# Kernel optimization log

Hardware: AMD Instinct MI355X
Metric: run time of the kernel (lower is better)

Reference implementation:

```python
import jax, jax.numpy as jnp
import numpy as np

T, B, N, C, H, D = 4, 8, 1024, 512, 8, 64
EPS = 1e-5


def setup_inputs() -> dict:
    key = jax.random.key(0)
    ks = jax.random.split(key, 16)
    d = {"x": jax.random.normal(ks[0], (T, B, N, C), jnp.float32)}
    for i, nm in enumerate(["q", "k", "v", "p"]):
        kW, kmu, kvar = jax.random.split(ks[1 + i], 3)
        d[f"W{nm}"] = jax.random.normal(kW, (C, C), jnp.float32) * 0.02
        d[f"b{nm}"] = jnp.zeros((C,), jnp.float32)
        d[f"g{nm}"] = jnp.ones((C,), jnp.float32)
        d[f"beta{nm}"] = jnp.zeros((C,), jnp.float32)
        d[f"mu{nm}"] = jax.random.normal(kmu, (C,), jnp.float32) * 0.1
        d[f"var{nm}"] = jax.random.uniform(kvar, (C,), jnp.float32, 0.5, 1.5)
    return d


def _lin_bn(z, W, b, g, beta, mu, var):
    # nn.Linear over channel dim, then eval-mode BatchNorm1d per channel
    y = jnp.einsum('tbnc,dc->tbnd', z, W) + b
    return (y - mu) * (g * jax.lax.rsqrt(var + EPS)) + beta


def _to_heads(z):
    # (t,b,n,c) -> (t,b,h,n,d)
    return z.reshape(T, B, N, H, D).transpose(0, 1, 3, 2, 4)


def reference(x, Wq, bq, gq, betaq, muq, varq,
              Wk, bk, gk, betak, muk, vark,
              Wv, bv, gv, betav, muv, varv,
              Wp, bp, gp, betap, mup, varp):
    q = _to_heads(_lin_bn(x, Wq, bq, gq, betaq, muq, varq))
    k = _to_heads(_lin_bn(x, Wk, bk, gk, betak, muk, vark))
    v = _to_heads(_lin_bn(x, Wv, bv, gv, betav, muv, varv))
    # attention_linear variant: kv = (k^T @ v) / N ; y = q @ kv
    kv = jnp.einsum('tbhnd,tbhne->tbhde', k, v) / float(N)  # (t,b,h,d,d)
    y = jnp.einsum('tbhnd,tbhde->tbhne', q, kv)             # (t,b,h,n,d)
    y = y.transpose(0, 1, 3, 2, 4).reshape(T, B, N, C)
    return _lin_bn(y, Wp, bp, gp, betap, mup, varp)
```

## Files before the change

### kernel.cpp

```cpp
#include <hip/hip_runtime.h>

#define T_ 4
#define B_ 8
#define N_ 1024
#define C_ 512
#define H_ 8
#define D_ 64
#define M_ (T_*B_*N_)
#define TB_ (T_*B_)

typedef __bf16 bf16;
typedef __bf16 bf16x4 __attribute__((ext_vector_type(4)));
typedef __bf16 bf16x8 __attribute__((ext_vector_type(8)));
typedef float f32x4 __attribute__((ext_vector_type(4)));

__device__ __forceinline__ void gload16(const void* g, void* l) {
  __builtin_amdgcn_global_load_lds(
      (const __attribute__((address_space(1))) void*)g,
      (__attribute__((address_space(3))) void*)l, 16, 0, 0);
}

struct PtrPack { const float* p[24]; };

__global__ __launch_bounds__(256)
void prep_m(PtrPack pk, bf16* __restrict__ WB, float* __restrict__ BS,
            bf16* __restrict__ WqT) {
  const int t = threadIdx.x;
  if (blockIdx.x < 2048) {
    const int mat = blockIdx.x >> 9, d = blockIdx.x & 511;
    const float* W    = pk.p[6*mat + 0];
    const float* b    = pk.p[6*mat + 1];
    const float* g    = pk.p[6*mat + 2];
    const float* beta = pk.p[6*mat + 3];
    const float* mu   = pk.p[6*mat + 4];
    const float* var  = pk.p[6*mat + 5];
    float s = g[d] * rsqrtf(var[d] + 1e-5f);
    if (t == 0) BS[mat*512 + d] = (b[d] - mu[d]) * s + beta[d];
    bf16* Wout = WB + (size_t)mat * 262144 + (size_t)d * 512;
    for (int c = t; c < 512; c += 256)
      Wout[c] = (bf16)(W[(size_t)d * 512 + c] * s);
    return;
  }
  const int e = blockIdx.x - 2048;
  const int di = e >> 3, ci = e & 7;
  __shared__ float lds[64][65];
  const float* W = pk.p[0];
  const float* g = pk.p[2];
  const float* var = pk.p[5];
  const int rgrp = t >> 4, k = t & 15;
#pragma unroll
  for (int p = 0; p < 4; p++) {
    int r = p * 16 + rgrp;
    int d = di * 64 + r;
    float s = g[d] * rsqrtf(var[d] + 1e-5f);
    float4 v = *(const float4*)(W + (size_t)d * 512 + ci * 64 + k * 4);
    lds[r][k*4+0] = v.x * s; lds[r][k*4+1] = v.y * s;
    lds[r][k*4+2] = v.z * s; lds[r][k*4+3] = v.w * s;
  }
  __syncthreads();
#pragma unroll
  for (int p = 0; p < 16; p++) {
    int c = p * 4 + (t >> 6), dd = t & 63;
    WqT[(size_t)(ci*64 + c) * 512 + di*64 + dd] = (bf16)lds[dd][c];
  }
}

__global__ __launch_bounds__(256)
void cvt_x_t(const float* __restrict__ x, bf16* __restrict__ xb,
             bf16* __restrict__ xT, float* __restrict__ spart) {
  const int bid = blockIdx.x;
  const int tb = bid >> 7, nc = (bid >> 3) & 15, cc = bid & 7;
  const int t = threadIdx.x;
  __shared__ float lds[64][65];
  __shared__ float sred[16][64];
  const float* xbase = x + (size_t)tb * 524288 + (size_t)nc * 64 * 512 + cc * 64;
  bf16* xbb = xb + (size_t)tb * 524288 + (size_t)nc * 64 * 512 + cc * 64;
  bf16* xTb = xT + (size_t)tb * 524288 + (size_t)(cc * 64) * 1024 + nc * 64;
  const int rgrp = t >> 4, k = t & 15;
  float s0 = 0, s1 = 0, s2 = 0, s3 = 0;
#pragma unroll
  for (int p = 0; p < 4; p++) {
    int r = p * 16 + rgrp;
    float4 v = *(const float4*)(xbase + (size_t)r * 512 + k * 4);
    bf16x4 o; o[0]=(bf16)v.x; o[1]=(bf16)v.y; o[2]=(bf16)v.z; o[3]=(bf16)v.w;
    *(bf16x4*)(xbb + (size_t)r * 512 + k * 4) = o;
    lds[r][k*4+0]=v.x; lds[r][k*4+1]=v.y; lds[r][k*4+2]=v.z; lds[r][k*4+3]=v.w;
    s0 += v.x; s1 += v.y; s2 += v.z; s3 += v.w;
  }
  sred[rgrp][k*4+0]=s0; sred[rgrp][k*4+1]=s1; sred[rgrp][k*4+2]=s2; sred[rgrp][k*4+3]=s3;
  __syncthreads();
#pragma unroll
  for (int p = 0; p < 16; p++) {
    int c = p * 4 + (t >> 6), n = t & 63;
    xTb[(size_t)c * 1024 + n] = (bf16)lds[n][c];
  }
  if (t < 64) {
    float tot = 0;
#pragma unroll
    for (int rg = 0; rg < 16; rg++) tot += sred[rg][t];
    spart[(size_t)((tb*8 + cc)*16 + nc) * 64 + t] = tot;
  }
}

__global__ __launch_bounds__(256)
void gram_ksvs(const bf16* __restrict__ xT, const bf16* __restrict__ WB,
               const float* __restrict__ spart, bf16* __restrict__ Gb,
               float* __restrict__ ksv) {
  const int t = threadIdx.x;
  __shared__ __align__(16) char smem[24576];
  if (blockIdx.x >= 640) {
    const int e = blockIdx.x - 640, tb = e >> 1, m = e & 1;
    float* sl = (float*)smem;
#pragma unroll
    for (int half = 0; half < 2; half++) {
      int c = t + half * 256, cc = c >> 6, cl = c & 63;
      float tot = 0;
#pragma unroll
      for (int ncf = 0; ncf < 16; ncf++)
        tot += spart[(size_t)((tb*8 + cc)*16 + ncf) * 64 + cl];
      sl[c] = tot;
    }
    __syncthreads();
#pragma unroll
    for (int half = 0; half < 2; half++) {
      int d = t + half * 256;
      const bf16* Wrow = WB + (size_t)(m + 1) * 262144 + (size_t)d * 512;
      float acc = 0;
      for (int k = 0; k < 512; k += 8) {
        bf16x8 wv = *(const bf16x8*)(Wrow + k);
#pragma unroll
        for (int i = 0; i < 8; i++) acc += (float)wv[i] * sl[k + i];
      }
      ksv[m * 16384 + tb * 512 + d] = acc;
    }
    return;
  }
  constexpr int K = 1024;
  const int bid = blockIdx.x;
  const int xcd = bid & 7, j9 = bid >> 3;
  const int bat = xcd + 8 * (j9 / 20);
  const int tile = j9 % 20;
  int mi, ni;
  if (tile < 8)       { mi = tile;          ni = 0; }
  else if (tile < 14) { mi = tile - 8 + 2;  ni = 1; }
  else if (tile < 18) { mi = tile - 14 + 4; ni = 2; }
  else                { mi = tile - 18 + 6; ni = 3; }
  const bf16* A = xT + (size_t)bat * 524288;
  const int m0 = mi * 64, n0 = ni * 128;
  bf16* As = (bf16*)smem;
  bf16* Bs = (bf16*)(smem + 8192);
  const int w = t >> 6, l = t & 63;
  const int wm = w >> 1, wn = w & 1;
  const int lr = l & 15, lq = l >> 4, l7 = l & 7, lh = l >> 3;
  const int srcc = (l7 ^ lh) * 8;
  f32x4 acc[2][4] = {};
  for (int kt = 0; kt < 16; kt++) {
#pragma unroll
    for (int i = 0; i < 2; i++) {
      int rb = w * 16 + i * 8;
      gload16(A + (size_t)(m0 + rb + lh) * K + kt * 64 + srcc, &As[rb * 64]);
    }
#pragma unroll
    for (int i = 0; i < 4; i++) {
      int rb = w * 32 + i * 8;
      gload16(A + (size_t)(n0 + rb + lh) * K + kt * 64 + srcc, &Bs[rb * 64]);
    }
    __syncthreads();
    bf16x8 af[2][2], bv[4][2];
#pragma unroll
    for (int f = 0; f < 2; f++) {
      int ra = wm * 32 + f * 16 + lr;
#pragma unroll
      for (int s = 0; s < 2; s++)
        af[f][s] = *(const bf16x8*)&As[ra * 64 + (((s*4+lq) ^ (ra & 7)) * 8)];
    }
#pragma unroll
    for (int f = 0; f < 4; f++) {
      int rb2 = wn * 64 + f * 16 + lr;
#pragma unroll
      for (int s = 0; s < 2; s++)
        bv[f][s] = *(const bf16x8*)&Bs[rb2 * 64 + (((s*4+lq) ^ (rb2 & 7)) * 8)];
    }
#pragma unroll
    for (int mt = 0; mt < 2; mt++)
#pragma unroll
      for (int nt = 0; nt < 4; nt++)
#pragma unroll
        for (int s = 0; s < 2; s++)
          acc[mt][nt] = __builtin_amdgcn_mfma_f32_16x16x32_bf16(
              af[mt][s], bv[nt][s], acc[mt][nt], 0, 0, 0);
    __syncthreads();
  }
  bf16* ob = Gb + (size_t)bat * 262144;
#pragma unroll
  for (int mt = 0; mt < 2; mt++)
#pragma unroll
    for (int nt = 0; nt < 4; nt++) {
      int j = n0 + wn * 64 + nt * 16 + lr;
      size_t mrow = (size_t)m0 + wm * 32 + mt * 16 + lq * 4;
#pragma unroll
      for (int r = 0; r < 4; r++)
        ob[(mrow + r) * 512 + j] = (bf16)acc[mt][nt][r];
    }
  bf16* TB = (bf16*)smem;
#pragma unroll
  for (int mt = 0; mt < 2; mt++)
#pragma unroll
    for (int nt = 0; nt < 4; nt++) {
      int a = wn * 64 + nt * 16 + lr;
#pragma unroll
      for (int r = 0; r < 4; r++) {
        int b = wm * 32 + mt * 16 + lq * 4 + r;
        TB[(a * 64 + b) ^ ((a & 7) << 3)] = (bf16)acc[mt][nt][r];
      }
    }
  __syncthreads();
  const int rowa = t >> 1, half = t & 1;
#pragma unroll
  for (int i = 0; i < 4; i++) {
    int c8 = half * 4 + i;
    bf16x8 v = *(const bf16x8*)&TB[(rowa * 64 + c8 * 8) ^ ((rowa & 7) << 3)];
    *(bf16x8*)(ob + (size_t)(n0 + rowa) * 512 + m0 + c8 * 8) = v;
  }
}

template <int NKT, int MTILES, bool BF16OUT, bool BIAS>
__global__ __launch_bounds__(256, 6)
void gemm_n(const bf16* __restrict__ Abase, size_t Astr,
            const bf16* __restrict__ Btbase, size_t Btstr,
            const float* __restrict__ BSb, const float* __restrict__ cpart,
            bf16* __restrict__ ob, float* __restrict__ of, size_t Ostr) {
  constexpr int K = NKT * 64;
  constexpr int PERB = MTILES * 4;
  const int bid = blockIdx.x;
  const int xcd = bid & 7, j9 = bid >> 3;
  const int bat = xcd + 8 * (j9 / PERB);
  const int tile = j9 % PERB;
  const int mi = tile >> 2, ni = tile & 3;
  const bf16* A = Abase + (size_t)bat * Astr;
  const bf16* Bt = Btbase + (size_t)bat * Btstr;
  const int m0 = mi * 64, n0 = ni * 128;
  __shared__ __align__(16) bf16 As[64][64];
  __shared__ __align__(16) bf16 Bs[128][64];
  const int tid = threadIdx.x, w = tid >> 6, l = tid & 63;
  const int wm = w >> 1, wn = w & 1;
  const int lr = l & 15, lq = l >> 4, l7 = l & 7, lh = l >> 3;
  const int srcc = (l7 ^ lh) * 8;
  f32x4 acc[2][4] = {};
  for (int kt = 0; kt < NKT; kt++) {
#pragma unroll
    for (int i = 0; i < 2; i++) {
      int rb = w * 16 + i * 8;
      gload16(A + (size_t)(m0 + rb + lh) * K + kt * 64 + srcc, &As[rb][0]);
    }
#pragma unroll
    for (int i = 0; i < 4; i++) {
      int rb = w * 32 + i * 8;
      gload16(Bt + (size_t)(n0 + rb + lh) * K + kt * 64 + srcc, &Bs[rb][0]);
    }
    __syncthreads();
    bf16x8 af[2][2], bv[4][2];
#pragma unroll
    for (int f = 0; f < 2; f++) {
      int ra = wm * 32 + f * 16 + lr;
#pragma unroll
      for (int s = 0; s < 2; s++)
        af[f][s] = *(const bf16x8*)&As[ra][((s*4+lq) ^ (ra & 7)) * 8];
    }
#pragma unroll
    for (int f = 0; f < 4; f++) {
      int rb2 = wn * 64 + f * 16 + lr;
#pragma unroll
      for (int s = 0; s < 2; s++)
        bv[f][s] = *(const bf16x8*)&Bs[rb2][((s*4+lq) ^ (rb2 & 7)) * 8];
    }
#pragma unroll
    for (int mt = 0; mt < 2; mt++)
#pragma unroll
      for (int nt = 0; nt < 4; nt++)
#pragma unroll
        for (int s = 0; s < 2; s++)
          acc[mt][nt] = __builtin_amdgcn_mfma_f32_16x16x32_bf16(
              af[mt][s], bv[nt][s], acc[mt][nt], 0, 0, 0);
    __syncthreads();
  }

  float bja[4];
  if constexpr (BIAS) {
#pragma unroll
    for (int nt = 0; nt < 4; nt++) {
      int j = n0 + wn * 64 + nt * 16 + lr;
      float bj = BSb[1536 + j];
#pragma unroll
      for (int h = 0; h < 8; h++)
        bj += cpart[(size_t)(bat * 8 + h) * 512 + j];
      bja[nt] = bj;
    }
  }
#pragma unroll
  for (int mt = 0; mt < 2; mt++)
#pragma unroll
    for (int nt = 0; nt < 4; nt++) {
      int j = n0 + wn * 64 + nt * 16 + lr;
      size_t mrow = (size_t)m0 + wm * 32 + mt * 16 + lq * 4;
#pragma unroll
      for (int r = 0; r < 4; r++) {
        if constexpr (BF16OUT)
          ob[(size_t)bat * Ostr + (mrow + r) * 512 + j] = (bf16)acc[mt][nt][r];
        else
          of[(size_t)bat * Ostr + (mrow + r) * 512 + j] =
              acc[mt][nt][r] + (BIAS ? bja[nt] : 0.f);
      }
    }
}

__global__ __launch_bounds__(256)
void kvz(const bf16* __restrict__ KGb, const bf16* __restrict__ WB,
         const float* __restrict__ BS, const float* __restrict__ ksv,
         bf16* __restrict__ ZT, float* __restrict__ cpart) {
  const int gid = blockIdx.x, tb = gid >> 3, h = gid & 7;
  const int t = threadIdx.x, w = t >> 6, l = t & 63;
  const int lr = l & 15, lq = l >> 4;
  __shared__ __align__(16) char lds[65536 + 65536 + 8192];
  bf16* bufA = (bf16*)lds;
  bf16* bufV = (bf16*)(lds + 65536);
  bf16* kvb  = (bf16*)(lds + 131072);

#pragma unroll
  for (int i = 0; i < 16; i++) {
    int r = i * 4 + w;
    gload16(KGb + (size_t)tb * 262144 + (size_t)(64*h + r) * 512 + ((l ^ (r & 7)) * 8),
            bufA + r * 512);
    gload16(WB + 2u * 262144 + (size_t)(64*h + r) * 512 + ((l ^ (r & 7)) * 8),
            bufV + r * 512);
  }
  __syncthreads();

  f32x4 acc2[4][4] = {};
#pragma unroll
  for (int ks = 0; ks < 4; ks++) {
    int gch = w * 16 + ks * 4 + lq;
    bf16x8 af2[4], bv2[4];
#pragma unroll
    for (int mf = 0; mf < 4; mf++) {
      int d = mf * 16 + lr;
      af2[mf] = *(const bf16x8*)&bufA[d * 512 + ((gch ^ (d & 7)) * 8)];
    }
#pragma unroll
    for (int nf = 0; nf < 4; nf++) {
      int e = nf * 16 + lr;
      bv2[nf] = *(const bf16x8*)&bufV[e * 512 + ((gch ^ (e & 7)) * 8)];
    }
#pragma unroll
    for (int mf = 0; mf < 4; mf++)
#pragma unroll
      for (int nf = 0; nf < 4; nf++)
        acc2[mf][nf] = __builtin_amdgcn_mfma_f32_16x16x32_bf16(
            af2[mf], bv2[nf], acc2[mf][nf], 0, 0, 0);
  }
  __syncthreads();

  float* part = (float*)lds + w * 4096;
#pragma unroll
  for (int mf = 0; mf < 4; mf++)
#pragma unroll
    for (int nf = 0; nf < 4; nf++)
#pragma unroll
      for (int r = 0; r < 4; r++) {
        int d = mf * 16 + lq * 4 + r, e = nf * 16 + lr;
        part[d * 64 + e] = acc2[mf][nf][r];
      }
  __syncthreads();
  {
    const float inv = 1.f / 1024.f;
    const float* pb = (const float*)lds;
#pragma unroll
    for (int jj = 0; jj < 16; jj++) {
      int flat = jj * 256 + t, d = flat >> 6, e = flat & 63;
      float s = pb[flat] + pb[4096 + flat] + pb[8192 + flat] + pb[12288 + flat];
      float ksh = ksv[tb * 512 + 64*h + d];
      float vsh = ksv[16384 + tb * 512 + 64*h + e];
      float bkh = BS[512 + 64*h + d];
      float bvh = BS[1024 + 64*h + e];
      float kv = (s + ksh * bvh + bkh * vsh) * inv + bkh * bvh;
      kvb[d * 64 + (((e >> 3) ^ (d & 7)) * 8 + (e & 7))] = (bf16)kv;
    }
  }
  __syncthreads();

#pragma unroll
  for (int i = 0; i < 16; i++) {
    int rb = i * 32 + w * 8;
    int r = rb + (l >> 3);
    gload16(WB + 3u * 262144 + (size_t)r * 512 + 64*h + (((l & 7) ^ (r & 7)) * 8),
            bufA + rb * 64);
  }
  __syncthreads();

  f32x4 acc3[4][8] = {};
#pragma unroll
  for (int s = 0; s < 2; s++) {
    bf16x8 af3[4];
#pragma unroll
    for (int mf = 0; mf < 4; mf++) {
      int d = mf * 16 + lr;
      af3[mf] = *(const bf16x8*)&kvb[d * 64 + (((s*4+lq) ^ (d & 7)) * 8)];
    }
#pragma unroll
    for (int nf = 0; nf < 8; nf++) {
      int jj = w * 128 + nf * 16 + lr;
      bf16x8 b3 = *(const bf16x8*)&bufA[jj * 64 + (((s*4+lq) ^ (jj & 7)) * 8)];
#pragma unroll
      for (int mf = 0; mf < 4; mf++)
        acc3[mf][nf] = __builtin_amdgcn_mfma_f32_16x16x32_bf16(
            af3[mf], b3, acc3[mf][nf], 0, 0, 0);
    }
  }

  bf16* zbase = ZT + (size_t)tb * 262144 + 64*h;
#pragma unroll
  for (int nf = 0; nf < 8; nf++) {
    int jj = w * 128 + nf * 16 + lr;
    float cp = 0.f;
#pragma unroll
    for (int mf = 0; mf < 4; mf++) {
      bf16x4 o;
#pragma unroll
      for (int r = 0; r < 4; r++) {
        o[r] = (bf16)acc3[mf][nf][r];
        cp += acc3[mf][nf][r] * BS[64*h + mf*16 + lq*4 + r];
      }
      *(bf16x4*)(zbase + (size_t)jj * 512 + mf * 16 + lq * 4) = o;
    }
    cp += __shfl_xor(cp, 16);
    cp += __shfl_xor(cp, 32);
    if (lq == 0) cpart[(size_t)(tb * 8 + h) * 512 + jj] = cp;
  }
}

extern "C" void kernel_launch(void* const* d_in, const int* in_sizes, int n_in,
                              void* d_out, int out_size, void* d_ws, size_t ws_size,
                              hipStream_t stream) {
  const float* x = (const float*)d_in[0];
  char* ws = (char*)d_ws;
  bf16*  xb    = (bf16*)(ws + 0);
  bf16*  xT    = (bf16*)(ws + 33554432);
  bf16*  Gb    = (bf16*)(ws + 67108864);
  bf16*  KGb   = (bf16*)(ws + 83886080);
  bf16*  ZT    = (bf16*)(ws + 100663296);
  bf16*  VT    = (bf16*)(ws + 117440512);
  bf16*  WB    = (bf16*)(ws + 134217728);
  bf16*  WqT   = (bf16*)(ws + 136314880);
  float* BS    = (float*)(ws + 136839168);
  float* ksv   = (float*)(ws + 136847360);
  float* cpart = (float*)(ws + 136978432);
  float* spart = (float*)(ws + 137502720);
  (void)in_sizes; (void)n_in; (void)out_size; (void)ws_size;

  PtrPack pk;
  for (int i = 0; i < 24; i++) pk.p[i] = (const float*)d_in[1 + i];

  prep_m<<<2112, 256, 0, stream>>>(pk, WB, BS, WqT);
  cvt_x_t<<<4096, 256, 0, stream>>>(x, xb, xT, spart);
  gram_ksvs<<<704, 256, 0, stream>>>(xT, WB, spart, Gb, ksv);
  gemm_n<8, 8, true, false><<<1024, 256, 0, stream>>>(
      WB + 262144, 0, Gb, 262144, nullptr, nullptr, KGb, nullptr, 262144);
  kvz<<<256, 256, 0, stream>>>(KGb, WB, BS, ksv, ZT, cpart);
  gemm_n<8, 8, true, false><<<1024, 256, 0, stream>>>(
      ZT, 262144, WqT, 0, nullptr, nullptr, VT, nullptr, 262144);
  gemm_n<8, 16, false, true><<<2048, 256, 0, stream>>>(
      xb, 524288, VT, 262144, BS, cpart, nullptr, (float*)d_out, 524288);
}
```

Before: 134.6 us.

## Merge prep kernels, precompute output bias vector, and drop LDS staging in kvz

Merges the weight-prep and x-conversion kernels into one launch, which removes a launch and lets the two independent jobs run side by side. Adds a dedicated ZT×WqT GEMM kernel whose extra blocks precompute the per-batch output bias, so the final GEMM reads one bias value per column instead of summing eight partials. kvz now reads K/V and Wp fragments straight from global memory with a different per-wave split, removing large LDS staging and the cross-wave reduction. The cost is uncached strided global reads in kvz, which may lower memory efficiency there.

```diff
diff --git a/kernel.cpp b/kernel.cpp
--- a/kernel.cpp
+++ b/kernel.cpp
@@ -23,11 +23,51 @@
 struct PtrPack { const float* p[24]; };
 
 __global__ __launch_bounds__(256)
-void prep_m(PtrPack pk, bf16* __restrict__ WB, float* __restrict__ BS,
-            bf16* __restrict__ WqT) {
+void cvt_prep(PtrPack pk, const float* __restrict__ x, bf16* __restrict__ xb,
+              bf16* __restrict__ xT, float* __restrict__ spart,
+              bf16* __restrict__ WB, float* __restrict__ BS,
+              bf16* __restrict__ WqT) {
   const int t = threadIdx.x;
-  if (blockIdx.x < 2048) {
-    const int mat = blockIdx.x >> 9, d = blockIdx.x & 511;
+  __shared__ __align__(16) char smem[21120];
+  if (blockIdx.x < 4096) {
+    const int bid = blockIdx.x;
+    const int tb = bid >> 7, nc = (bid >> 3) & 15, cc = bid & 7;
+    float* lds = (float*)smem;
+    float* sred = (float*)smem + 4160;
+    const float* xbase = x + (size_t)tb * 524288 + (size_t)nc * 64 * 512 + cc * 64;
+    bf16* xbb = xb + (size_t)tb * 524288 + (size_t)nc * 64 * 512 + cc * 64;
+    bf16* xTb = xT + (size_t)tb * 524288 + (size_t)(cc * 64) * 1024 + nc * 64;
+    const int rgrp = t >> 4, k = t & 15;
+    float s0 = 0, s1 = 0, s2 = 0, s3 = 0;
+#pragma unroll
+    for (int p = 0; p < 4; p++) {
+      int r = p * 16 + rgrp;
+      float4 v = *(const float4*)(xbase + (size_t)r * 512 + k * 4);
+      bf16x4 o; o[0]=(bf16)v.x; o[1]=(bf16)v.y; o[2]=(bf16)v.z; o[3]=(bf16)v.w;
+      *(bf16x4*)(xbb + (size_t)r * 512 + k * 4) = o;
+      lds[r*65 + k*4+0]=v.x; lds[r*65 + k*4+1]=v.y;
+      lds[r*65 + k*4+2]=v.z; lds[r*65 + k*4+3]=v.w;
+      s0 += v.x; s1 += v.y; s2 += v.z; s3 += v.w;
+    }
+    sred[rgrp*64 + k*4+0]=s0; sred[rgrp*64 + k*4+1]=s1;
+    sred[rgrp*64 + k*4+2]=s2; sred[rgrp*64 + k*4+3]=s3;
+    __syncthreads();
+#pragma unroll
+    for (int p = 0; p < 16; p++) {
+      int c = p * 4 + (t >> 6), n = t & 63;
+      xTb[(size_t)c * 1024 + n] = (bf16)lds[n*65 + c];
+    }
+    if (t < 64) {
+      float tot = 0;
+#pragma unroll
+      for (int rg = 0; rg < 16; rg++) tot += sred[rg*64 + t];
+      spart[(size_t)((tb*8 + cc)*16 + nc) * 64 + t] = tot;
+    }
+    return;
+  }
+  if (blockIdx.x < 6144) {
+    const int e = blockIdx.x - 4096;
+    const int mat = e >> 9, d = e & 511;
     const float* W    = pk.p[6*mat + 0];
     const float* b    = pk.p[6*mat + 1];
     const float* g    = pk.p[6*mat + 2];
@@ -41,9 +81,9 @@
       Wout[c] = (bf16)(W[(size_t)d * 512 + c] * s);
     return;
   }
-  const int e = blockIdx.x - 2048;
+  const int e = blockIdx.x - 6144;
   const int di = e >> 3, ci = e & 7;
-  __shared__ float lds[64][65];
+  float* lds = (float*)smem;
   const float* W = pk.p[0];
   const float* g = pk.p[2];
   const float* var = pk.p[5];
@@ -54,51 +94,14 @@
     int d = di * 64 + r;
     float s = g[d] * rsqrtf(var[d] + 1e-5f);
     float4 v = *(const float4*)(W + (size_t)d * 512 + ci * 64 + k * 4);
-    lds[r][k*4+0] = v.x * s; lds[r][k*4+1] = v.y * s;
-    lds[r][k*4+2] = v.z * s; lds[r][k*4+3] = v.w * s;
+    lds[r*65 + k*4+0] = v.x * s; lds[r*65 + k*4+1] = v.y * s;
+    lds[r*65 + k*4+2] = v.z * s; lds[r*65 + k*4+3] = v.w * s;
   }
   __syncthreads();
 #pragma unroll
   for (int p = 0; p < 16; p++) {
     int c = p * 4 + (t >> 6), dd = t & 63;
-    WqT[(size_t)(ci*64 + c) * 512 + di*64 + dd] = (bf16)lds[dd][c];
-  }
-}
-
-__global__ __launch_bounds__(256)
-void cvt_x_t(const float* __restrict__ x, bf16* __restrict__ xb,
-             bf16* __restrict__ xT, float* __restrict__ spart) {
-  const int bid = blockIdx.x;
-  const int tb = bid >> 7, nc = (bid >> 3) & 15, cc = bid & 7;
-  const int t = threadIdx.x;
-  __shared__ float lds[64][65];
-  __shared__ float sred[16][64];
-  const float* xbase = x + (size_t)tb * 524288 + (size_t)nc * 64 * 512 + cc * 64;
-  bf16* xbb = xb + (size_t)tb * 524288 + (size_t)nc * 64 * 512 + cc * 64;
-  bf16* xTb = xT + (size_t)tb * 524288 + (size_t)(cc * 64) * 1024 + nc * 64;
-  const int rgrp = t >> 4, k = t & 15;
-  float s0 = 0, s1 = 0, s2 = 0, s3 = 0;
-#pragma unroll
-  for (int p = 0; p < 4; p++) {
-    int r = p * 16 + rgrp;
-    float4 v = *(const float4*)(xbase + (size_t)r * 512 + k * 4);
-    bf16x4 o; o[0]=(bf16)v.x; o[1]=(bf16)v.y; o[2]=(bf16)v.z; o[3]=(bf16)v.w;
-    *(bf16x4*)(xbb + (size_t)r * 512 + k * 4) = o;
-    lds[r][k*4+0]=v.x; lds[r][k*4+1]=v.y; lds[r][k*4+2]=v.z; lds[r][k*4+3]=v.w;
-    s0 += v.x; s1 += v.y; s2 += v.z; s3 += v.w;
-  }
-  sred[rgrp][k*4+0]=s0; sred[rgrp][k*4+1]=s1; sred[rgrp][k*4+2]=s2; sred[rgrp][k*4+3]=s3;
-  __syncthreads();
-#pragma unroll
-  for (int p = 0; p < 16; p++) {
-    int c = p * 4 + (t >> 6), n = t & 63;
-    xTb[(size_t)c * 1024 + n] = (bf16)lds[n][c];
-  }
-  if (t < 64) {
-    float tot = 0;
-#pragma unroll
-    for (int rg = 0; rg < 16; rg++) tot += sred[rg][t];
-    spart[(size_t)((tb*8 + cc)*16 + nc) * 64 + t] = tot;
+    WqT[(size_t)(ci*64 + c) * 512 + di*64 + dd] = (bf16)lds[dd*65 + c];
   }
 }
 
@@ -228,7 +231,7 @@
 __global__ __launch_bounds__(256, 6)
 void gemm_n(const bf16* __restrict__ Abase, size_t Astr,
             const bf16* __restrict__ Btbase, size_t Btstr,
-            const float* __restrict__ BSb, const float* __restrict__ cpart,
+            const float* __restrict__ BSb,
             bf16* __restrict__ ob, float* __restrict__ of, size_t Ostr) {
   constexpr int K = NKT * 64;
   constexpr int PERB = MTILES * 4;
@@ -290,11 +293,7 @@
 #pragma unroll
     for (int nt = 0; nt < 4; nt++) {
       int j = n0 + wn * 64 + nt * 16 + lr;
-      float bj = BSb[1536 + j];
-#pragma unroll
-      for (int h = 0; h < 8; h++)
-        bj += cpart[(size_t)(bat * 8 + h) * 512 + j];
-      bja[nt] = bj;
+      bja[nt] = BSb[(size_t)bat * 512 + j];
     }
   }
 #pragma unroll
@@ -314,6 +313,87 @@
     }
 }
 
+__global__ __launch_bounds__(256, 6)
+void gemm_vtc(const bf16* __restrict__ ZT, const bf16* __restrict__ WqT,
+              const float* __restrict__ BS, const float* __restrict__ cpart,
+              bf16* __restrict__ VT, float* __restrict__ cvec) {
+  constexpr int K = 512;
+  const int tid = threadIdx.x;
+  if (blockIdx.x >= 1024) {
+    const int tb = blockIdx.x - 1024;
+#pragma unroll
+    for (int half = 0; half < 2; half++) {
+      int j = tid + half * 256;
+      float s = BS[1536 + j];
+#pragma unroll
+      for (int h = 0; h < 8; h++) s += cpart[(size_t)(tb * 8 + h) * 512 + j];
+      cvec[tb * 512 + j] = s;
+    }
+    return;
+  }
+  const int bid = blockIdx.x;
+  const int xcd = bid & 7, j9 = bid >> 3;
+  const int bat = xcd + 8 * (j9 >> 5);
+  const int tile = j9 & 31;
+  const int mi = tile >> 2, ni = tile & 3;
+  const bf16* A = ZT + (size_t)bat * 262144;
+  const int m0 = mi * 64, n0 = ni * 128;
+  __shared__ __align__(16) bf16 As[64][64];
+  __shared__ __align__(16) bf16 Bs[128][64];
+  const int w = tid >> 6, l = tid & 63;
+  const int wm = w >> 1, wn = w & 1;
+  const int lr = l & 15, lq = l >> 4, l7 = l & 7, lh = l >> 3;
+  const int srcc = (l7 ^ lh) * 8;
+  f32x4 acc[2][4] = {};
+  for (int kt = 0; kt < 8; kt++) {
+#pragma unroll
+    for (int i = 0; i < 2; i++) {
+      int rb = w * 16 + i * 8;
+      gload16(A + (size_t)(m0 + rb + lh) * K + kt * 64 + srcc, &As[rb][0]);
+    }
+#pragma unroll
+    for (int i = 0; i < 4; i++) {
+      int rb = w * 32 + i * 8;
+      gload16(WqT + (size_t)(n0 + rb + lh) * K + kt * 64 + srcc, &Bs[rb][0]);
+    }
+    __syncthreads();
+    bf16x8 af[2][2], bv[4][2];
+#pragma unroll
+    for (int f = 0; f < 2; f++) {
+      int ra = wm * 32 + f * 16 + lr;
+#pragma unroll
+      for (int s = 0; s < 2; s++)
+        af[f][s] = *(const bf16x8*)&As[ra][((s*4+lq) ^ (ra & 7)) * 8];
+    }
+#pragma unroll
+    for (int f = 0; f < 4; f++) {
+      int rb2 = wn * 64 + f * 16 + lr;
+#pragma unroll
+      for (int s = 0; s < 2; s++)
+        bv[f][s] = *(const bf16x8*)&Bs[rb2][((s*4+lq) ^ (rb2 & 7)) * 8];
+    }
+#pragma unroll
+    for (int mt = 0; mt < 2; mt++)
+#pragma unroll
+      for (int nt = 0; nt < 4; nt++)
+#pragma unroll
+        for (int s = 0; s < 2; s++)
+          acc[mt][nt] = __builtin_amdgcn_mfma_f32_16x16x32_bf16(
+              af[mt][s], bv[nt][s], acc[mt][nt], 0, 0, 0);
+    __syncthreads();
+  }
+#pragma unroll
+  for (int mt = 0; mt < 2; mt++)
+#pragma unroll
+    for (int nt = 0; nt < 4; nt++) {
+      int j = n0 + wn * 64 + nt * 16 + lr;
+      size_t mrow = (size_t)m0 + wm * 32 + mt * 16 + lq * 4;
+#pragma unroll
+      for (int r = 0; r < 4; r++)
+        VT[(size_t)bat * 262144 + (mrow + r) * 512 + j] = (bf16)acc[mt][nt][r];
+    }
+}
+
 __global__ __launch_bounds__(256)
 void kvz(const bf16* __restrict__ KGb, const bf16* __restrict__ WB,
          const float* __restrict__ BS, const float* __restrict__ ksv,
@@ -321,79 +401,36 @@
   const int gid = blockIdx.x, tb = gid >> 3, h = gid & 7;
   const int t = threadIdx.x, w = t >> 6, l = t & 63;
   const int lr = l & 15, lq = l >> 4;
-  __shared__ __align__(16) char lds[65536 + 65536 + 8192];
-  bf16* bufA = (bf16*)lds;
-  bf16* bufV = (bf16*)(lds + 65536);
-  bf16* kvb  = (bf16*)(lds + 131072);
-
-#pragma unroll
-  for (int i = 0; i < 16; i++) {
-    int r = i * 4 + w;
-    gload16(KGb + (size_t)tb * 262144 + (size_t)(64*h + r) * 512 + ((l ^ (r & 7)) * 8),
-            bufA + r * 512);
-    gload16(WB + 2u * 262144 + (size_t)(64*h + r) * 512 + ((l ^ (r & 7)) * 8),
-            bufV + r * 512);
-  }
-  __syncthreads();
-
-  f32x4 acc2[4][4] = {};
-#pragma unroll
-  for (int ks = 0; ks < 4; ks++) {
-    int gch = w * 16 + ks * 4 + lq;
-    bf16x8 af2[4], bv2[4];
+  __shared__ __align__(16) bf16 kvb[4096];
+
+  const bf16* KGrow = KGb + (size_t)tb * 262144 + (size_t)(64*h) * 512;
+  const bf16* Vrow  = WB + 2u * 262144 + (size_t)(64*h) * 512;
+
+  f32x4 acc2[4] = {};
+  for (int ks = 0; ks < 16; ks++) {
+    const int kc = ks * 32 + lq * 8;
+    bf16x8 bv = *(const bf16x8*)(Vrow + (size_t)(w*16 + lr) * 512 + kc);
 #pragma unroll
     for (int mf = 0; mf < 4; mf++) {
-      int d = mf * 16 + lr;
-      af2[mf] = *(const bf16x8*)&bufA[d * 512 + ((gch ^ (d & 7)) * 8)];
-    }
-#pragma unroll
-    for (int nf = 0; nf < 4; nf++) {
-      int e = nf * 16 + lr;
-      bv2[nf] = *(const bf16x8*)&bufV[e * 512 + ((gch ^ (e & 7)) * 8)];
-    }
-#pragma unroll
-    for (int mf = 0; mf < 4; mf++)
-#pragma unroll
-      for (int nf = 0; nf < 4; nf++)
-        acc2[mf][nf] = __builtin_amdgcn_mfma_f32_16x16x32_bf16(
-            af2[mf], bv2[nf], acc2[mf][nf], 0, 0, 0);
-  }
-  __syncthreads();
-
-  float* part = (float*)lds + w * 4096;
-#pragma unroll
-  for (int mf = 0; mf < 4; mf++)
-#pragma unroll
-    for (int nf = 0; nf < 4; nf++)
-#pragma unroll
-      for (int r = 0; r < 4; r++) {
-        int d = mf * 16 + lq * 4 + r, e = nf * 16 + lr;
-        part[d * 64 + e] = acc2[mf][nf][r];
-      }
-  __syncthreads();
+      bf16x8 af = *(const bf16x8*)(KGrow + (size_t)(mf*16 + lr) * 512 + kc);
+      acc2[mf] = __builtin_amdgcn_mfma_f32_16x16x32_bf16(af, bv, acc2[mf], 0, 0, 0);
+    }
+  }
   {
     const float inv = 1.f / 1024.f;
-    const float* pb = (const float*)lds;
-#pragma unroll
-    for (int jj = 0; jj < 16; jj++) {
-      int flat = jj * 256 + t, d = flat >> 6, e = flat & 63;
-      float s = pb[flat] + pb[4096 + flat] + pb[8192 + flat] + pb[12288 + flat];
-      float ksh = ksv[tb * 512 + 64*h + d];
-      float vsh = ksv[16384 + tb * 512 + 64*h + e];
-      float bkh = BS[512 + 64*h + d];
-      float bvh = BS[1024 + 64*h + e];
-      float kv = (s + ksh * bvh + bkh * vsh) * inv + bkh * bvh;
-      kvb[d * 64 + (((e >> 3) ^ (d & 7)) * 8 + (e & 7))] = (bf16)kv;
-    }
-  }
-  __syncthreads();
-
-#pragma unroll
-  for (int i = 0; i < 16; i++) {
-    int rb = i * 32 + w * 8;
-    int r = rb + (l >> 3);
-    gload16(WB + 3u * 262144 + (size_t)r * 512 + 64*h + (((l & 7) ^ (r & 7)) * 8),
-            bufA + rb * 64);
+    const int e = w * 16 + lr;
+    const float vsh = ksv[16384 + tb * 512 + 64*h + e];
+    const float bvh = BS[1024 + 64*h + e];
+#pragma unroll
+    for (int mf = 0; mf < 4; mf++)
+#pragma unroll
+      for (int r = 0; r < 4; r++) {
+        int d = mf * 16 + lq * 4 + r;
+        float ksh = ksv[tb * 512 + 64*h + d];
+        float bkh = BS[512 + 64*h + d];
+        float kv = (acc2[mf][r] + ksh * bvh + bkh * vsh) * inv + bkh * bvh;
+        kvb[d * 64 + ((((e >> 3) ^ (d & 7)) * 8) + (e & 7))] = (bf16)kv;
+      }
   }
   __syncthreads();
 
@@ -409,7 +446,8 @@
 #pragma unroll
     for (int nf = 0; nf < 8; nf++) {
       int jj = w * 128 + nf * 16 + lr;
-      bf16x8 b3 = *(const bf16x8*)&bufA[jj * 64 + (((s*4+lq) ^ (jj & 7)) * 8)];
+      bf16x8 b3 = *(const bf16x8*)(WB + 3u * 262144 + (size_t)jj * 512 +
+                                   64*h + s * 32 + lq * 8);
 #pragma unroll
       for (int mf = 0; mf < 4; mf++)
         acc3[mf][nf] = __builtin_amdgcn_mfma_f32_16x16x32_bf16(
@@ -454,20 +492,19 @@
   float* BS    = (float*)(ws + 136839168);
   float* ksv   = (float*)(ws + 136847360);
   float* cpart = (float*)(ws + 136978432);
-  float* spart = (float*)(ws + 137502720);
+  float* cvec  = (float*)(ws + 137502720);
+  float* spart = (float*)(ws + 137568256);
   (void)in_sizes; (void)n_in; (void)out_size; (void)ws_size;
 
   PtrPack pk;
   for (int i = 0; i < 24; i++) pk.p[i] = (const float*)d_in[1 + i];
 
-  prep_m<<<2112, 256, 0, stream>>>(pk, WB, BS, WqT);
-  cvt_x_t<<<4096, 256, 0, stream>>>(x, xb, xT, spart);
+  cvt_prep<<<6208, 256, 0, stream>>>(pk, x, xb, xT, spart, WB, BS, WqT);
   gram_ksvs<<<704, 256, 0, stream>>>(xT, WB, spart, Gb, ksv);
   gemm_n<8, 8, true, false><<<1024, 256, 0, stream>>>(
-      WB + 262144, 0, Gb, 262144, nullptr, nullptr, KGb, nullptr, 262144);
+      WB + 262144, 0, Gb, 262144, nullptr, KGb, nullptr, 262144);
   kvz<<<256, 256, 0, stream>>>(KGb, WB, BS, ksv, ZT, cpart);
-  gemm_n<8, 8, true, false><<<1024, 256, 0, stream>>>(
-      ZT, 262144, WqT, 0, nullptr, nullptr, VT, nullptr, 262144);
+  gemm_vtc<<<1056, 256, 0, stream>>>(ZT, WqT, BS, cpart, VT, cvec);
   gemm_n<8, 16, false, true><<<2048, 256, 0, stream>>>(
-      xb, 524288, VT, 262144, BS, cpart, nullptr, (float*)d_out, 524288);
-}
+      xb, 524288, VT, 262144, cvec, nullptr, (float*)d_out, 524288);
+}
```

After: 135.7 us. Within noise of the previous version (+0.8%).
